# Kernel optimization log

Hardware: AMD Instinct MI355X
Metric: run time of the kernel (lower is better)

## Reference

```python
import jax, jax.numpy as jnp
import numpy as np

B, T, C = 8, 2048, 1024


def setup_inputs() -> dict:
    key = jax.random.key(0)
    ks = jax.random.split(key, 7)
    s = 0.02  # typical init scale for weights
    return {
        "x": jax.random.normal(ks[0], (B, T, C), jnp.float32),
        "wq": jax.random.normal(ks[1], (C, C), jnp.float32) * s,
        "bq": jax.random.normal(ks[2], (C,), jnp.float32) * s,
        "wk": jax.random.normal(ks[3], (C, C), jnp.float32) * s,
        "bk": jax.random.normal(ks[4], (C,), jnp.float32) * s,
        "wv": jax.random.normal(ks[5], (C, C), jnp.float32) * s,
        "bv": jax.random.normal(ks[6], (C,), jnp.float32) * s,
    }


def reference(x, wq, bq, wk, bk, wv, bv):
    # x: [B, T, C]; torch Linear stores weight as [out, in] -> x @ W.T + b
    Bx, Tx, Cx = x.shape
    Q = x @ wq.T + bq  # [B, T, C]
    K = x @ wk.T + bk
    V = x @ wv.T + bv
    # NOTE: source computes K @ Q^T (keys index rows, queries index columns)
    scores = jnp.einsum("btc,bsc->bts", K, Q) / jnp.sqrt(jnp.float32(Cx))  # [B, T, T]
    causal = jnp.tril(jnp.ones((Tx, Tx), dtype=bool))  # mask==0 above diagonal
    scores = jnp.where(causal, scores, -jnp.inf)
    # torch masked_fill with a (1,1,T,T) mask broadcasts scores to (1,B,T,T)
    scores = scores[None]  # [1, B, T, T]
    w = jax.nn.softmax(scores, axis=-1)
    out = jnp.einsum("abts,bsc->abtc", w, V)  # [1, B, T, C]
    return out
```

## Files before the change

kernel.cpp:

```cpp
#include <hip/hip_runtime.h>
#include <stdint.h>

typedef unsigned short u16;
typedef __attribute__((ext_vector_type(8))) __bf16 bf16x8;
typedef __attribute__((ext_vector_type(4))) float f32x4;

#define DEVI __device__ __forceinline__

DEVI u16 f32_to_bf16(float f) {
  uint32_t u = __builtin_bit_cast(uint32_t, f);
  u += 0x7FFFu + ((u >> 16) & 1u);
  return (u16)(u >> 16);
}

DEVI float bf16_to_f32(u16 h) {
  uint32_t u = ((uint32_t)h) << 16;
  return __builtin_bit_cast(float, u);
}

DEVI void gl2lds16(const void* g, void* l) {
  __builtin_amdgcn_global_load_lds(
      (const __attribute__((address_space(1))) void*)g,
      (__attribute__((address_space(3))) void*)l, 16, 0, 0);
}

#define SMEM_U16 17408

DEVI void gemm_bt_mainloop(const u16* __restrict__ A, const u16* __restrict__ B,
                           int lda, int ldb, int kIters,
                           u16* As, u16* Bs, f32x4 (&acc)[4][4]) {
  const int tid = threadIdx.x;
  const int lane = tid & 63;
  const int wid = tid >> 6;
  const int wr = wid >> 1, wc = wid & 1;
  const int l15 = lane & 15, quad = lane >> 4;

  const int srow = tid >> 3;
  const int sgrp = ((tid & 7) - srow) & 7;
  const u16* Ag = A + (size_t)srow * lda + sgrp * 8;
  const u16* Bg = B + (size_t)srow * ldb + sgrp * 8;
  char* AsDst = (char*)As + tid * 16;
  char* BsDst = (char*)Bs + tid * 16;

  const int a_row0 = wr * 64 + l15;
  const int b_row0 = wc * 64 + l15;

  for (int kb = 0; kb < kIters; ++kb) {
#pragma unroll
    for (int r = 0; r < 4; ++r) {
      gl2lds16(Ag + (size_t)(r * 32) * lda, AsDst + r * 4096);
      gl2lds16(Bg + (size_t)(r * 32) * ldb, BsDst + r * 4096);
    }
    Ag += 64;
    Bg += 64;
    __syncthreads();
#pragma unroll
    for (int kk = 0; kk < 2; ++kk) {
      const int gA = ((kk * 4 + quad + a_row0) & 7) * 8;
      const int gB = ((kk * 4 + quad + b_row0) & 7) * 8;
      bf16x8 af[4], bfr[4];
#pragma unroll
      for (int i = 0; i < 4; ++i)
        af[i] = *(const bf16x8*)(As + (a_row0 + i * 16) * 64 + gA);
#pragma unroll
      for (int j = 0; j < 4; ++j)
        bfr[j] = *(const bf16x8*)(Bs + (b_row0 + j * 16) * 64 + gB);
#pragma unroll
      for (int i = 0; i < 4; ++i)
#pragma unroll
        for (int j = 0; j < 4; ++j)
          acc[i][j] = __builtin_amdgcn_mfma_f32_16x16x32_bf16(af[i], bfr[j],
                                                              acc[i][j], 0, 0, 0);
    }
    __syncthreads();
  }
}

DEVI void store_tile_bf16(const u16* tile, u16* __restrict__ out, int ld_out) {
  const int tid = threadIdx.x;
  const int c0 = (tid & 15) * 8;
#pragma unroll
  for (int rr = 0; rr < 8; ++rr) {
    const int row = rr * 16 + (tid >> 4);
    const uint4 v = *(const uint4*)(tile + row * 136 + c0);
    *(uint4*)(out + (size_t)row * ld_out + c0) = v;
  }
}

__global__ void cast_f32_to_bf16_kernel(const float* __restrict__ src,
                                        u16* __restrict__ dst, int n4) {
  int i = blockIdx.x * blockDim.x + threadIdx.x;
  const int stride = gridDim.x * blockDim.x;
  for (; i < n4; i += stride) {
    const float4 v = ((const float4*)src)[i];
    ushort4 o;
    o.x = f32_to_bf16(v.x);
    o.y = f32_to_bf16(v.y);
    o.z = f32_to_bf16(v.z);
    o.w = f32_to_bf16(v.w);
    ((ushort4*)dst)[i] = o;
  }
}

__global__ void cast_w_kernel(const float* __restrict__ wq,
                              const float* __restrict__ wk,
                              const float* __restrict__ wv,
                              u16* __restrict__ wb) {
  const int z = blockIdx.y;
  const float* src = (z == 0) ? wq : (z == 1) ? wk : wv;
  u16* dst = wb + (size_t)z * 1048576;
  int i = blockIdx.x * blockDim.x + threadIdx.x;
  const int stride = gridDim.x * blockDim.x;
  for (; i < 262144; i += stride) {
    const float4 v = ((const float4*)src)[i];
    ushort4 o;
    o.x = f32_to_bf16(v.x);
    o.y = f32_to_bf16(v.y);
    o.z = f32_to_bf16(v.z);
    o.w = f32_to_bf16(v.w);
    ((ushort4*)dst)[i] = o;
  }
}

__global__ __launch_bounds__(256) void qkv_kernel(
    const u16* __restrict__ xb, const u16* __restrict__ wb,
    const float* __restrict__ bq, const float* __restrict__ bk,
    const float* __restrict__ bv, u16* __restrict__ Qb, u16* __restrict__ Kb,
    u16* __restrict__ Vt) {
  __shared__ __align__(16) u16 smem[SMEM_U16];
  u16* As = smem;
  u16* Bs = smem + 8192;

  const int id = blockIdx.x;
  const int xcd = id & 7;
  const int local = id >> 3;
  const int chunk = local >> 6;
  const int li = local & 63;
  const int x = (chunk % 3) * 8 + (li & 7);
  const int y = xcd * 16 + (chunk / 3) * 8 + (li >> 3);
  const int m0 = y * 128;
  const int z = x >> 3;
  const int n0 = (x & 7) * 128;
  const float* bias = (z == 0) ? bq : (z == 1) ? bk : bv;

  f32x4 acc[4][4];
#pragma unroll
  for (int i = 0; i < 4; ++i)
#pragma unroll
    for (int j = 0; j < 4; ++j) acc[i][j] = (f32x4){0.f, 0.f, 0.f, 0.f};

  gemm_bt_mainloop(xb + (size_t)m0 * 1024, wb + (size_t)(x * 128) * 1024, 1024,
                   1024, 16, As, Bs, acc);

  const int tid = threadIdx.x;
  const int lane = tid & 63, wid = tid >> 6;
  const int wr = wid >> 1, wc = wid & 1;
  const int l15 = lane & 15, quad = lane >> 4;

  if (z < 2) {
#pragma unroll
    for (int j = 0; j < 4; ++j) {
      const int col = wc * 64 + j * 16 + l15;
      const float bb = bias[n0 + col];
#pragma unroll
      for (int i = 0; i < 4; ++i) {
        const int row = wr * 64 + i * 16 + quad * 4;
#pragma unroll
        for (int r = 0; r < 4; ++r)
          smem[(row + r) * 136 + col] = f32_to_bf16(acc[i][j][r] + bb);
      }
    }
    __syncthreads();
    u16* Out = ((z == 0) ? Qb : Kb) + (size_t)m0 * 1024 + n0;
    store_tile_bf16(smem, Out, 1024);
  } else {
#pragma unroll
    for (int j = 0; j < 4; ++j) {
      const int c = wc * 64 + j * 16 + l15;
      const float bb = bias[n0 + c];
#pragma unroll
      for (int i = 0; i < 4; ++i) {
        const int t = wr * 64 + i * 16 + quad * 4;
        ushort4 o;
        o.x = f32_to_bf16(acc[i][j][0] + bb);
        o.y = f32_to_bf16(acc[i][j][1] + bb);
        o.z = f32_to_bf16(acc[i][j][2] + bb);
        o.w = f32_to_bf16(acc[i][j][3] + bb);
        *(ushort4*)(smem + c * 136 + t) = o;
      }
    }
    __syncthreads();
    const int bidx = m0 >> 11;
    const int t0 = m0 & 2047;
    u16* Out = Vt + ((size_t)bidx * 1024 + n0) * 2048 + t0;
    store_tile_bf16(smem, Out, 2048);
  }
}

__global__ __launch_bounds__(256) void score_kernel(const u16* __restrict__ Kb,
                                                    const u16* __restrict__ Qb,
                                                    u16* __restrict__ S) {
  const int b = blockIdx.x & 7;
  const int l = 135 - (blockIdx.x >> 3);
  int rt = (int)((sqrtf(8.f * l + 1.f) - 1.f) * 0.5f);
  int ct = l - rt * (rt + 1) / 2;
  if (ct > rt) { ++rt; ct = l - rt * (rt + 1) / 2; }
  if (ct < 0)  { --rt; ct = l - rt * (rt + 1) / 2; }

  __shared__ __align__(16) u16 smem[SMEM_U16];
  u16* As = smem;
  u16* Bs = smem + 8192;

  f32x4 acc[4][4];
#pragma unroll
  for (int i = 0; i < 4; ++i)
#pragma unroll
    for (int j = 0; j < 4; ++j) acc[i][j] = (f32x4){0.f, 0.f, 0.f, 0.f};

  const u16* A = Kb + ((size_t)b * 2048 + rt * 128) * 1024;
  const u16* B = Qb + ((size_t)b * 2048 + ct * 128) * 1024;
  gemm_bt_mainloop(A, B, 1024, 1024, 16, As, Bs, acc);

  const int tid = threadIdx.x;
  const int lane = tid & 63, wid = tid >> 6;
  const int wr = wid >> 1, wc = wid & 1;
  const int l15 = lane & 15, quad = lane >> 4;
  const bool diag = (rt == ct);

#pragma unroll
  for (int j = 0; j < 4; ++j) {
    const int col = wc * 64 + j * 16 + l15;
#pragma unroll
    for (int i = 0; i < 4; ++i) {
      const int row = wr * 64 + i * 16 + quad * 4;
#pragma unroll
      for (int r = 0; r < 4; ++r) {
        float e = __expf(acc[i][j][r] * 0.03125f);
        if (diag && col > row + r) e = 0.f;
        smem[(row + r) * 136 + col] = f32_to_bf16(e);
      }
    }
  }
  __syncthreads();
  u16* Out = S + ((size_t)b * 2048 + rt * 128) * 2048 + ct * 128;
  store_tile_bf16(smem, Out, 2048);
}

__global__ __launch_bounds__(256) void rowsum_kernel(const u16* __restrict__ S,
                                                     float* __restrict__ inv) {
  const int b = blockIdx.x & 7;
  const int t = blockIdx.x >> 3;
  const u16* row = S + ((size_t)b * 2048 + t) * 2048;
  const int nchunk = ((t >> 7) + 1) << 4;
  const int tid = threadIdx.x;

  float sum = 0.f;
  if (tid < nchunk) {
    const uint4 v = *(const uint4*)(row + tid * 8);
    const uint32_t w[4] = {v.x, v.y, v.z, v.w};
#pragma unroll
    for (int k = 0; k < 4; ++k) {
      sum += __builtin_bit_cast(float, w[k] << 16);
      sum += __builtin_bit_cast(float, w[k] & 0xFFFF0000u);
    }
  }
#pragma unroll
  for (int off = 32; off > 0; off >>= 1) sum += __shfl_down(sum, off);
  __shared__ float red[4];
  if ((tid & 63) == 0) red[tid >> 6] = sum;
  __syncthreads();
  if (tid == 0)
    inv[(size_t)b * 2048 + t] = 1.0f / (red[0] + red[1] + red[2] + red[3]);
}

__global__ __launch_bounds__(256) void pv_kernel(const u16* __restrict__ S,
                                                 const u16* __restrict__ Vt,
                                                 const float* __restrict__ inv,
                                                 float* __restrict__ Out) {
  const int b = blockIdx.x & 7;
  const int local = 127 - (blockIdx.x >> 3);
  const int rt = local >> 3;
  const int ct = local & 7;

  __shared__ __align__(16) u16 smem[SMEM_U16];
  u16* As = smem;
  u16* Bs = smem + 8192;
  float* ftile = (float*)smem;

  f32x4 acc[4][4];
#pragma unroll
  for (int i = 0; i < 4; ++i)
#pragma unroll
    for (int j = 0; j < 4; ++j) acc[i][j] = (f32x4){0.f, 0.f, 0.f, 0.f};

  const u16* A = S + (size_t)b * 2048 * 2048 + (size_t)(rt * 128) * 2048;
  const u16* B = Vt + (size_t)b * 1024 * 2048 + (size_t)(ct * 128) * 2048;
  gemm_bt_mainloop(A, B, 2048, 2048, (rt + 1) * 2, As, Bs, acc);

  const int tid = threadIdx.x;
  const int lane = tid & 63, wid = tid >> 6;
  const int wr = wid >> 1, wc = wid & 1;
  const int l15 = lane & 15, quad = lane >> 4;

  const float* invb = inv + (size_t)b * 2048 + rt * 128;
  float* Ob = Out + (size_t)b * 2048 * 1024 + (size_t)(rt * 128) * 1024 +
              ct * 128;
#pragma unroll
  for (int h = 0; h < 2; ++h) {
    if (wr == h) {
#pragma unroll
      for (int j = 0; j < 4; ++j) {
        const int col = wc * 64 + j * 16 + l15;
#pragma unroll
        for (int i = 0; i < 4; ++i) {
          const int row = i * 16 + quad * 4;
#pragma unroll
          for (int r = 0; r < 4; ++r)
            ftile[(row + r) * 132 + col] = acc[i][j][r];
        }
      }
    }
    __syncthreads();
#pragma unroll
    for (int rr = 0; rr < 8; ++rr) {
      const int row = rr * 8 + (tid >> 5);
      const int c0 = (tid & 31) * 4;
      const float iv = invb[h * 64 + row];
      float4 v = *(const float4*)(ftile + row * 132 + c0);
      v.x *= iv; v.y *= iv; v.z *= iv; v.w *= iv;
      *(float4*)(Ob + (size_t)(h * 64 + row) * 1024 + c0) = v;
    }
    __syncthreads();
  }
}

extern "C" void kernel_launch(void* const* d_in, const int* in_sizes, int n_in,
                              void* d_out, int out_size, void* d_ws,
                              size_t ws_size, hipStream_t stream) {
  const float* x = (const float*)d_in[0];
  const float* wq = (const float*)d_in[1];
  const float* bq = (const float*)d_in[2];
  const float* wk = (const float*)d_in[3];
  const float* bk = (const float*)d_in[4];
  const float* wv = (const float*)d_in[5];
  const float* bv = (const float*)d_in[6];
  float* out = (float*)d_out;
  char* ws = (char*)d_ws;

  u16* Qb = (u16*)(ws);
  u16* Kb = (u16*)(ws + ((size_t)32 << 20));
  u16* Vt = (u16*)(ws + ((size_t)64 << 20));
  u16* S = (u16*)(ws + ((size_t)96 << 20));
  u16* xb = (u16*)(ws + ((size_t)96 << 20));
  u16* wb = (u16*)(ws + ((size_t)128 << 20));
  float* inv = (float*)(ws);

  cast_f32_to_bf16_kernel<<<16384, 256, 0, stream>>>(x, xb, 16777216 / 4);
  cast_w_kernel<<<dim3(512, 3), 256, 0, stream>>>(wq, wk, wv, wb);

  qkv_kernel<<<3072, 256, 0, stream>>>(xb, wb, bq, bk, bv, Qb, Kb, Vt);

  score_kernel<<<8 * 136, 256, 0, stream>>>(Kb, Qb, S);

  rowsum_kernel<<<16384, 256, 0, stream>>>(S, inv);

  pv_kernel<<<8 * 128, 256, 0, stream>>>(S, Vt, inv, out);
}
```

Measured before the change: 349.9 us.

## Fuse row sums into score kernel via atomics and pack causal scores

Removes the separate rowsum kernel by accumulating exp row sums inside the score kernel with shuffle reductions and atomicAdd into a buffer zeroed by the weight-cast kernel. Scores are stored in a packed lower-triangular layout, which shrinks the S buffer and its write/read traffic. Several GEMMs swap operand roles, giving transposed epilogues with vectorized bias loads and the normalization folded into the PV accumulator write. Atomics add contention, and the float summation order becomes nondeterministic.

```diff
diff --git a/kernel.cpp b/kernel.cpp
--- a/kernel.cpp
+++ b/kernel.cpp
@@ -13,11 +13,6 @@
   return (u16)(u >> 16);
 }
 
-DEVI float bf16_to_f32(u16 h) {
-  uint32_t u = ((uint32_t)h) << 16;
-  return __builtin_bit_cast(float, u);
-}
-
 DEVI void gl2lds16(const void* g, void* l) {
   __builtin_amdgcn_global_load_lds(
       (const __attribute__((address_space(1))) void*)g,
@@ -25,6 +20,8 @@
 }
 
 #define SMEM_U16 17408
+
+#define S_BATCH 2228224
 
 DEVI void gemm_bt_mainloop(const u16* __restrict__ A, const u16* __restrict__ B,
                            int lda, int ldb, int kIters,
@@ -105,8 +102,13 @@
 __global__ void cast_w_kernel(const float* __restrict__ wq,
                               const float* __restrict__ wk,
                               const float* __restrict__ wv,
-                              u16* __restrict__ wb) {
+                              u16* __restrict__ wb, float* __restrict__ sums) {
   const int z = blockIdx.y;
+  if (z == 3) {
+    int i = blockIdx.x * blockDim.x + threadIdx.x;
+    if (i < 4096) ((float4*)sums)[i] = (float4){0.f, 0.f, 0.f, 0.f};
+    return;
+  }
   const float* src = (z == 0) ? wq : (z == 1) ? wk : wv;
   u16* dst = wb + (size_t)z * 1048576;
   int i = blockIdx.x * blockDim.x + threadIdx.x;
@@ -149,31 +151,35 @@
 #pragma unroll
     for (int j = 0; j < 4; ++j) acc[i][j] = (f32x4){0.f, 0.f, 0.f, 0.f};
 
-  gemm_bt_mainloop(xb + (size_t)m0 * 1024, wb + (size_t)(x * 128) * 1024, 1024,
-                   1024, 16, As, Bs, acc);
-
   const int tid = threadIdx.x;
   const int lane = tid & 63, wid = tid >> 6;
   const int wr = wid >> 1, wc = wid & 1;
   const int l15 = lane & 15, quad = lane >> 4;
 
   if (z < 2) {
-#pragma unroll
-    for (int j = 0; j < 4; ++j) {
-      const int col = wc * 64 + j * 16 + l15;
-      const float bb = bias[n0 + col];
-#pragma unroll
-      for (int i = 0; i < 4; ++i) {
-        const int row = wr * 64 + i * 16 + quad * 4;
-#pragma unroll
-        for (int r = 0; r < 4; ++r)
-          smem[(row + r) * 136 + col] = f32_to_bf16(acc[i][j][r] + bb);
+    gemm_bt_mainloop(wb + (size_t)(x * 128) * 1024, xb + (size_t)m0 * 1024,
+                     1024, 1024, 16, As, Bs, acc);
+#pragma unroll
+    for (int i = 0; i < 4; ++i) {
+      const int c0 = wr * 64 + i * 16 + quad * 4;
+      const float4 b4 = *(const float4*)(bias + n0 + c0);
+#pragma unroll
+      for (int j = 0; j < 4; ++j) {
+        const int t = wc * 64 + j * 16 + l15;
+        ushort4 o;
+        o.x = f32_to_bf16(acc[i][j][0] + b4.x);
+        o.y = f32_to_bf16(acc[i][j][1] + b4.y);
+        o.z = f32_to_bf16(acc[i][j][2] + b4.z);
+        o.w = f32_to_bf16(acc[i][j][3] + b4.w);
+        *(ushort4*)(smem + t * 136 + c0) = o;
       }
     }
     __syncthreads();
     u16* Out = ((z == 0) ? Qb : Kb) + (size_t)m0 * 1024 + n0;
     store_tile_bf16(smem, Out, 1024);
   } else {
+    gemm_bt_mainloop(xb + (size_t)m0 * 1024, wb + (size_t)(x * 128) * 1024,
+                     1024, 1024, 16, As, Bs, acc);
 #pragma unroll
     for (int j = 0; j < 4; ++j) {
       const int c = wc * 64 + j * 16 + l15;
@@ -199,7 +205,8 @@
 
 __global__ __launch_bounds__(256) void score_kernel(const u16* __restrict__ Kb,
                                                     const u16* __restrict__ Qb,
-                                                    u16* __restrict__ S) {
+                                                    u16* __restrict__ Spk,
+                                                    float* __restrict__ sums) {
   const int b = blockIdx.x & 7;
   const int l = 135 - (blockIdx.x >> 3);
   int rt = (int)((sqrtf(8.f * l + 1.f) - 1.f) * 0.5f);
@@ -217,8 +224,8 @@
 #pragma unroll
     for (int j = 0; j < 4; ++j) acc[i][j] = (f32x4){0.f, 0.f, 0.f, 0.f};
 
-  const u16* A = Kb + ((size_t)b * 2048 + rt * 128) * 1024;
-  const u16* B = Qb + ((size_t)b * 2048 + ct * 128) * 1024;
+  const u16* A = Qb + ((size_t)b * 2048 + ct * 128) * 1024;
+  const u16* B = Kb + ((size_t)b * 2048 + rt * 128) * 1024;
   gemm_bt_mainloop(A, B, 1024, 1024, 16, As, Bs, acc);
 
   const int tid = threadIdx.x;
@@ -227,55 +234,47 @@
   const int l15 = lane & 15, quad = lane >> 4;
   const bool diag = (rt == ct);
 
+  float sj[4] = {0.f, 0.f, 0.f, 0.f};
+#pragma unroll
+  for (int i = 0; i < 4; ++i) {
+    const int s0 = wr * 64 + i * 16 + quad * 4;
+#pragma unroll
+    for (int j = 0; j < 4; ++j) {
+      const int t = wc * 64 + j * 16 + l15;
+      ushort4 o;
+      float e[4];
+#pragma unroll
+      for (int r = 0; r < 4; ++r) {
+        float v = __expf(acc[i][j][r] * 0.03125f);
+        if (diag && (s0 + r) > t) v = 0.f;
+        e[r] = v;
+        sj[j] += v;
+      }
+      o.x = f32_to_bf16(e[0]);
+      o.y = f32_to_bf16(e[1]);
+      o.z = f32_to_bf16(e[2]);
+      o.w = f32_to_bf16(e[3]);
+      *(ushort4*)(smem + t * 136 + s0) = o;
+    }
+  }
 #pragma unroll
   for (int j = 0; j < 4; ++j) {
-    const int col = wc * 64 + j * 16 + l15;
-#pragma unroll
-    for (int i = 0; i < 4; ++i) {
-      const int row = wr * 64 + i * 16 + quad * 4;
-#pragma unroll
-      for (int r = 0; r < 4; ++r) {
-        float e = __expf(acc[i][j][r] * 0.03125f);
-        if (diag && col > row + r) e = 0.f;
-        smem[(row + r) * 136 + col] = f32_to_bf16(e);
-      }
-    }
+    float v = sj[j];
+    v += __shfl_xor(v, 16);
+    v += __shfl_xor(v, 32);
+    if (quad == 0)
+      atomicAdd(&sums[(size_t)b * 2048 + rt * 128 + wc * 64 + j * 16 + l15], v);
   }
   __syncthreads();
-  u16* Out = S + ((size_t)b * 2048 + rt * 128) * 2048 + ct * 128;
-  store_tile_bf16(smem, Out, 2048);
-}
-
-__global__ __launch_bounds__(256) void rowsum_kernel(const u16* __restrict__ S,
-                                                     float* __restrict__ inv) {
-  const int b = blockIdx.x & 7;
-  const int t = blockIdx.x >> 3;
-  const u16* row = S + ((size_t)b * 2048 + t) * 2048;
-  const int nchunk = ((t >> 7) + 1) << 4;
-  const int tid = threadIdx.x;
-
-  float sum = 0.f;
-  if (tid < nchunk) {
-    const uint4 v = *(const uint4*)(row + tid * 8);
-    const uint32_t w[4] = {v.x, v.y, v.z, v.w};
-#pragma unroll
-    for (int k = 0; k < 4; ++k) {
-      sum += __builtin_bit_cast(float, w[k] << 16);
-      sum += __builtin_bit_cast(float, w[k] & 0xFFFF0000u);
-    }
-  }
-#pragma unroll
-  for (int off = 32; off > 0; off >>= 1) sum += __shfl_down(sum, off);
-  __shared__ float red[4];
-  if ((tid & 63) == 0) red[tid >> 6] = sum;
-  __syncthreads();
-  if (tid == 0)
-    inv[(size_t)b * 2048 + t] = 1.0f / (red[0] + red[1] + red[2] + red[3]);
-}
-
-__global__ __launch_bounds__(256) void pv_kernel(const u16* __restrict__ S,
+  const int ld = (rt + 1) * 128;
+  u16* Out = Spk + (size_t)b * S_BATCH + (size_t)(rt * (rt + 1) / 2) * 16384 +
+             ct * 128;
+  store_tile_bf16(smem, Out, ld);
+}
+
+__global__ __launch_bounds__(256) void pv_kernel(const u16* __restrict__ Spk,
                                                  const u16* __restrict__ Vt,
-                                                 const float* __restrict__ inv,
+                                                 const float* __restrict__ sums,
                                                  float* __restrict__ Out) {
   const int b = blockIdx.x & 7;
   const int local = 127 - (blockIdx.x >> 3);
@@ -293,30 +292,36 @@
 #pragma unroll
     for (int j = 0; j < 4; ++j) acc[i][j] = (f32x4){0.f, 0.f, 0.f, 0.f};
 
-  const u16* A = S + (size_t)b * 2048 * 2048 + (size_t)(rt * 128) * 2048;
-  const u16* B = Vt + (size_t)b * 1024 * 2048 + (size_t)(ct * 128) * 2048;
-  gemm_bt_mainloop(A, B, 2048, 2048, (rt + 1) * 2, As, Bs, acc);
+  const u16* A = Vt + ((size_t)b * 1024 + ct * 128) * 2048;
+  const u16* B = Spk + (size_t)b * S_BATCH +
+                 (size_t)(rt * (rt + 1) / 2) * 16384;
+  const int ldb = (rt + 1) * 128;
+  gemm_bt_mainloop(A, B, 2048, ldb, (rt + 1) * 2, As, Bs, acc);
 
   const int tid = threadIdx.x;
   const int lane = tid & 63, wid = tid >> 6;
   const int wr = wid >> 1, wc = wid & 1;
   const int l15 = lane & 15, quad = lane >> 4;
 
-  const float* invb = inv + (size_t)b * 2048 + rt * 128;
+  const float* sumsb = sums + (size_t)b * 2048 + rt * 128;
   float* Ob = Out + (size_t)b * 2048 * 1024 + (size_t)(rt * 128) * 1024 +
               ct * 128;
 #pragma unroll
   for (int h = 0; h < 2; ++h) {
-    if (wr == h) {
+    if (wc == h) {
 #pragma unroll
       for (int j = 0; j < 4; ++j) {
-        const int col = wc * 64 + j * 16 + l15;
+        const int tl = j * 16 + l15;
+        const float iv = 1.0f / sumsb[h * 64 + tl];
 #pragma unroll
         for (int i = 0; i < 4; ++i) {
-          const int row = i * 16 + quad * 4;
-#pragma unroll
-          for (int r = 0; r < 4; ++r)
-            ftile[(row + r) * 132 + col] = acc[i][j][r];
+          const int c0 = wr * 64 + i * 16 + quad * 4;
+          float4 v;
+          v.x = acc[i][j][0] * iv;
+          v.y = acc[i][j][1] * iv;
+          v.z = acc[i][j][2] * iv;
+          v.w = acc[i][j][3] * iv;
+          *(float4*)(ftile + tl * 132 + c0) = v;
         }
       }
     }
@@ -325,9 +330,7 @@
     for (int rr = 0; rr < 8; ++rr) {
       const int row = rr * 8 + (tid >> 5);
       const int c0 = (tid & 31) * 4;
-      const float iv = invb[h * 64 + row];
-      float4 v = *(const float4*)(ftile + row * 132 + c0);
-      v.x *= iv; v.y *= iv; v.z *= iv; v.w *= iv;
+      const float4 v = *(const float4*)(ftile + row * 132 + c0);
       *(float4*)(Ob + (size_t)(h * 64 + row) * 1024 + c0) = v;
     }
     __syncthreads();
@@ -350,19 +353,17 @@
   u16* Qb = (u16*)(ws);
   u16* Kb = (u16*)(ws + ((size_t)32 << 20));
   u16* Vt = (u16*)(ws + ((size_t)64 << 20));
-  u16* S = (u16*)(ws + ((size_t)96 << 20));
+  u16* Spk = (u16*)(ws + ((size_t)96 << 20));
   u16* xb = (u16*)(ws + ((size_t)96 << 20));
-  u16* wb = (u16*)(ws + ((size_t)128 << 20));
-  float* inv = (float*)(ws);
+  float* sums = (float*)(ws + ((size_t)132 << 20));
+  u16* wb = (u16*)(ws + ((size_t)134 << 20));
 
   cast_f32_to_bf16_kernel<<<16384, 256, 0, stream>>>(x, xb, 16777216 / 4);
-  cast_w_kernel<<<dim3(512, 3), 256, 0, stream>>>(wq, wk, wv, wb);
+  cast_w_kernel<<<dim3(512, 4), 256, 0, stream>>>(wq, wk, wv, wb, sums);
 
   qkv_kernel<<<3072, 256, 0, stream>>>(xb, wb, bq, bk, bv, Qb, Kb, Vt);
 
-  score_kernel<<<8 * 136, 256, 0, stream>>>(Kb, Qb, S);
-
-  rowsum_kernel<<<16384, 256, 0, stream>>>(S, inv);
-
-  pv_kernel<<<8 * 128, 256, 0, stream>>>(S, Vt, inv, out);
-}
+  score_kernel<<<8 * 136, 256, 0, stream>>>(Kb, Qb, Spk, sums);
+
+  pv_kernel<<<8 * 128, 256, 0, stream>>>(Spk, Vt, sums, out);
+}
```

Measured after the change: 344.5 us. Within noise of the previous version (-1.5%).
